# Kernel optimization log

Measured on AMD Instinct MI355X. Metric: run time of the kernel, lower is better.

The kernel has to match this reference:

```python
import jax, jax.numpy as jnp
import numpy as np

N = 100000      # n_nodes
E = 1600000     # n_edges (avg degree 16)
D_IN, D_H, D_OUT = 128, 64, 16


def setup_inputs() -> dict:
    key = jax.random.key(0)
    k1, k2, k3, k4 = jax.random.split(key, 4)
    x = jax.random.normal(k1, (N, D_IN), dtype=jnp.float32)
    edge_index = jax.random.randint(k2, (2, E), 0, N, dtype=jnp.int32)
    W1 = jax.random.normal(k3, (D_IN, D_H), dtype=jnp.float32) / np.sqrt(D_IN)
    b1 = jnp.zeros((D_H,), dtype=jnp.float32)
    W2 = jax.random.normal(k4, (D_H, D_OUT), dtype=jnp.float32) / np.sqrt(D_H)
    b2 = jnp.zeros((D_OUT,), dtype=jnp.float32)
    return {"x": x, "edge_index": edge_index, "W1": W1, "b1": b1, "W2": W2, "b2": b2}


def gcn_conv(x, src, dst, W, b, n):
    """PyG GCNConv: linear transform, then deg^-1/2 A deg^-1/2 aggregation, + bias.
    src/dst already include self-loops."""
    h = x @ W                                              # [n, d_out]
    deg = jax.ops.segment_sum(jnp.ones_like(dst, dtype=h.dtype), dst, num_segments=n)
    dinv = jnp.where(deg > 0, jax.lax.rsqrt(jnp.maximum(deg, 1.0)), 0.0)
    norm = dinv[src] * dinv[dst]                           # [E+n]
    msgs = h[src] * norm[:, None]                          # gather + scale
    out = jax.ops.segment_sum(msgs, dst, num_segments=n)   # scatter-add
    return out + b


def reference(x, edge_index, W1, b1, W2, b2):
    loops = jnp.arange(N, dtype=edge_index.dtype)
    src = jnp.concatenate([edge_index[0], loops])
    dst = jnp.concatenate([edge_index[1], loops])
    h = jax.nn.relu(gcn_conv(x, src, dst, W1, b1, N))
    return gcn_conv(h, src, dst, W2, b2, N)
```

## Files before the change

kernel.cpp:

```cpp
#include <hip/hip_runtime.h>
#include <cstdint>

#define N_NODES 100000
#define N_EDGES 1600000
#define D_IN    128
#define D_H     64
#define D_OUT   16
#define M_TILES 6250

#define NBKT   512
#define NPB    196
#define BCAP   4096
#define TILE_E 4096
#define NTILES ((N_EDGES + TILE_E - 1) / TILE_E)
#define G1     256
#define GEMM_BLOCKS ((M_TILES + 3) / 4)

typedef __attribute__((ext_vector_type(8))) short short8;
typedef __attribute__((ext_vector_type(4))) float floatx4;

static __device__ __forceinline__ unsigned short f2bf(float f) {
    unsigned int u = __float_as_uint(f);
    u = u + 0x7FFFu + ((u >> 16) & 1u);
    return (unsigned short)(u >> 16);
}
static __device__ __forceinline__ float bf2f(unsigned short h) {
    return __uint_as_float(((unsigned int)h) << 16);
}


__global__ __launch_bounds__(512) void zero_small_kernel(int* __restrict__ cursors,
                                                         int* __restrict__ srcs) {
    cursors[threadIdx.x] = 0;
    if (threadIdx.x < 16) srcs[N_EDGES + threadIdx.x] = 0;
}

__global__ __launch_bounds__(256) void fused_bin_gemm1_kernel(
        const int* __restrict__ src, const int* __restrict__ dst,
        int* __restrict__ cursors, int* __restrict__ region,
        const float* __restrict__ x, const float* __restrict__ W1,
        unsigned short* __restrict__ hs) {
    __shared__ int hcnt[NBKT];
    __shared__ int hbase[NBKT];
    __shared__ unsigned short bhi_lds[8192];
    __shared__ unsigned short blo_lds[8192];

    const int t = threadIdx.x;

    if (blockIdx.x < G1) {
        for (int tile = blockIdx.x; tile < NTILES; tile += G1) {
            for (int i = t; i < NBKT; i += 256) hcnt[i] = 0;
            __syncthreads();
            int e0 = tile * TILE_E + t * 16;
            int pk[16], bk[16], rk[16];
            bool full = (e0 + 16 <= N_EDGES);
            if (full) {
                const int4* dp = (const int4*)(dst + e0);
                const int4* sp = (const int4*)(src + e0);
                int dv[16], sv[16];
                #pragma unroll
                for (int q = 0; q < 4; ++q) {
                    int4 d4 = dp[q]; int4 s4 = sp[q];
                    dv[4*q+0]=d4.x; dv[4*q+1]=d4.y; dv[4*q+2]=d4.z; dv[4*q+3]=d4.w;
                    sv[4*q+0]=s4.x; sv[4*q+1]=s4.y; sv[4*q+2]=s4.z; sv[4*q+3]=s4.w;
                }
                #pragma unroll
                for (int k = 0; k < 16; ++k) {
                    int d = dv[k];
                    int b = d / NPB;
                    bk[k] = b;
                    pk[k] = ((d - b * NPB) << 17) | sv[k];
                    rk[k] = atomicAdd(&hcnt[b], 1);
                }
            }
            __syncthreads();
            for (int i = t; i < NBKT; i += 256) {
                int c = hcnt[i];
                if (c > 0) hbase[i] = atomicAdd(&cursors[i], c);
            }
            __syncthreads();
            if (full) {
                #pragma unroll
                for (int k = 0; k < 16; ++k)
                    region[bk[k] * BCAP + hbase[bk[k]] + rk[k]] = pk[k];
            }
            __syncthreads();
        }
        return;
    }

    for (int e = t; e < 8192; e += 256) {
        int j    = e & 7;
        int lane = (e >> 3) & 63;
        int pair = e >> 9;
        int kc   = pair >> 2;
        int nt   = pair & 3;
        int k = kc * 32 + (lane >> 4) * 8 + j;
        int n = nt * 16 + (lane & 15);
        float w = W1[k * D_H + n];
        unsigned short hi = f2bf(w);
        float lo = w - bf2f(hi);
        bhi_lds[e] = hi;
        blo_lds[e] = f2bf(lo);
    }
    __syncthreads();

    int wid  = t >> 6;
    int lane = t & 63;
    int quad = lane >> 4;
    int m    = lane & 15;

    int tile = (blockIdx.x - G1) * 4 + wid;
    if (tile >= M_TILES) return;
    int mbase = tile * 16;

    const float* xr = x + (size_t)(mbase + m) * D_IN + quad * 8;
    short8 ahi[4], alo[4];
    #pragma unroll
    for (int kc = 0; kc < 4; ++kc) {
        floatx4 v0 = *(const floatx4*)(xr + kc * 32);
        floatx4 v1 = *(const floatx4*)(xr + kc * 32 + 4);
        float f[8] = {v0.x, v0.y, v0.z, v0.w, v1.x, v1.y, v1.z, v1.w};
        #pragma unroll
        for (int j = 0; j < 8; ++j) {
            unsigned short hi = f2bf(f[j]);
            float lo = f[j] - bf2f(hi);
            ahi[kc][j] = (short)hi;
            alo[kc][j] = (short)f2bf(lo);
        }
    }

    floatx4 acc[4] = {{0.f,0.f,0.f,0.f},{0.f,0.f,0.f,0.f},{0.f,0.f,0.f,0.f},{0.f,0.f,0.f,0.f}};
    #pragma unroll
    for (int kc = 0; kc < 4; ++kc) {
        #pragma unroll
        for (int nt = 0; nt < 4; ++nt) {
            int fo = ((kc * 4 + nt) * 64 + lane) * 8;
            short8 bhi = *(const short8*)&bhi_lds[fo];
            short8 blo = *(const short8*)&blo_lds[fo];
            acc[nt] = __builtin_amdgcn_mfma_f32_16x16x32_bf16(ahi[kc], bhi, acc[nt], 0, 0, 0);
            acc[nt] = __builtin_amdgcn_mfma_f32_16x16x32_bf16(ahi[kc], blo, acc[nt], 0, 0, 0);
            acc[nt] = __builtin_amdgcn_mfma_f32_16x16x32_bf16(alo[kc], bhi, acc[nt], 0, 0, 0);
        }
    }

    #pragma unroll
    for (int nt = 0; nt < 4; ++nt) {
        int col = nt * 16 + m;
        #pragma unroll
        for (int r = 0; r < 4; ++r) {
            int row = mbase + quad * 4 + r;
            hs[row * D_H + col] = f2bf(acc[nt][r]);
        }
    }
}

__global__ __launch_bounds__(256) void build_kernel(const int* __restrict__ cursors,
                                                    const int* __restrict__ region,
                                                    int* __restrict__ offsets,
                                                    float* __restrict__ dinv,
                                                    int* __restrict__ srcs) {
    __shared__ int lhist[NPB];
    __shared__ int lscan[NPB + 1];
    __shared__ int sbuf[256];
    __shared__ int srt[BCAP];
    __shared__ int red[4];
    int b = blockIdx.x;
    int t = threadIdx.x;

    int c0 = cursors[t];
    int c1 = cursors[t + 256];
    int p = ((t < b) ? c0 : 0) + ((t + 256 < b) ? c1 : 0);
    int lane = t & 63, wid = t >> 6;
    #pragma unroll
    for (int off = 32; off > 0; off >>= 1) p += __shfl_down(p, off);
    if (lane == 0) red[wid] = p;
    __syncthreads();
    int base = red[0] + red[1] + red[2] + red[3];
    int cnt = cursors[b];
    const int* reg = region + b * BCAP;

    for (int i = t; i < NPB; i += 256) lhist[i] = 0;
    __syncthreads();
    for (int i = t; i < cnt; i += 256) {
        int ln = reg[i] >> 17;
        atomicAdd(&lhist[ln], 1);
    }
    __syncthreads();
    int v = (t < NPB) ? lhist[t] : 0;
    sbuf[t] = v;
    __syncthreads();
    for (int off = 1; off < 256; off <<= 1) {
        int u = (t >= off) ? sbuf[t - off] : 0;
        __syncthreads();
        sbuf[t] += u;
        __syncthreads();
    }
    int incl = sbuf[t];
    if (t < NPB) lscan[t] = incl - v;
    if (t == NPB - 1) lscan[NPB] = incl;
    __syncthreads();
    if (t < NPB) lhist[t] = incl - v;
    __syncthreads();

    int node0 = b * NPB;
    int nlim = N_NODES - node0;
    if (nlim > NPB) nlim = NPB;
    if (t < nlim) {
        offsets[node0 + t] = base + lscan[t];
        int c = lscan[t + 1] - lscan[t];
        dinv[node0 + t] = rsqrtf((float)c + 1.0f);
    }
    if (b == (N_NODES - 1) / NPB && t == 0) offsets[N_NODES] = base + cnt;

    for (int i = t; i < cnt; i += 256) {
        int pk = reg[i];
        int ln = pk >> 17;
        int pos = atomicAdd(&lhist[ln], 1);
        srt[pos] = pk & 0x1FFFF;
    }
    __syncthreads();
    for (int i = t; i < cnt; i += 256) srcs[base + i] = srt[i];
}

__global__ __launch_bounds__(256) void agg1_fused_kernel(const unsigned short* __restrict__ hs,
                                                         const int* __restrict__ offsets,
                                                         const int* __restrict__ srcs,
                                                         const float* __restrict__ dinv,
                                                         const float* __restrict__ b1,
                                                         const float* __restrict__ W2,
                                                         float* __restrict__ h2s) {
    __shared__ float w2t[16 * 68];
    __shared__ float rbuf[16 * 68];

    const int tid = threadIdx.x;
    for (int i = tid; i < 1024; i += 256) {
        int j = i >> 4, c = i & 15;
        w2t[c * 68 + j] = W2[i];
    }

    const int g    = tid >> 4;
    const int sl   = tid & 15;
    const int node = blockIdx.x * 16 + g;
    const int c4   = sl * 4;

    const int beg = offsets[node];
    const int end = offsets[node + 1];
    const float dv = dinv[node];

    ushort4 s4v = *(const ushort4*)(hs + (size_t)node * D_H + c4);
    float a0 = bf2f(s4v.x) * dv, a1 = bf2f(s4v.y) * dv;
    float a2 = bf2f(s4v.z) * dv, a3 = bf2f(s4v.w) * dv;

    for (int e = beg; e < end; e += 16) {
        int rem = end - e;
        int idx = srcs[e + sl];
        float dvv = dinv[idx];
        #pragma unroll
        for (int k = 0; k < 16; ++k) {
            int j   = __shfl(idx, k, 16);
            float dj = __shfl(dvv, k, 16);
            ushort4 v = *(const ushort4*)(hs + (size_t)j * D_H + c4);
            float m = (k < rem) ? dj : 0.0f;
            a0 = fmaf(bf2f(v.x), m, a0);
            a1 = fmaf(bf2f(v.y), m, a1);
            a2 = fmaf(bf2f(v.z), m, a2);
            a3 = fmaf(bf2f(v.w), m, a3);
        }
    }

    const floatx4 bb = *(const floatx4*)(b1 + c4);
    float* rb = rbuf + g * 68;
    rb[c4 + 0] = fmaxf(a0 * dv + bb.x, 0.f);
    rb[c4 + 1] = fmaxf(a1 * dv + bb.y, 0.f);
    rb[c4 + 2] = fmaxf(a2 * dv + bb.z, 0.f);
    rb[c4 + 3] = fmaxf(a3 * dv + bb.w, 0.f);
    __syncthreads();

    float p = 0.f;
    #pragma unroll
    for (int t4 = 0; t4 < 16; ++t4) {
        floatx4 rv = *(const floatx4*)(rb + 4 * t4);
        floatx4 wv = *(const floatx4*)(&w2t[sl * 68 + 4 * t4]);
        p += rv.x * wv.x + rv.y * wv.y + rv.z * wv.z + rv.w * wv.w;
    }
    h2s[node * D_OUT + sl] = p * dv;
}

__global__ __launch_bounds__(256) void agg2_kernel(const float* __restrict__ h2s,
                                                   const int* __restrict__ offsets,
                                                   const int* __restrict__ srcs,
                                                   const float* __restrict__ dinv,
                                                   const float* __restrict__ b2,
                                                   float* __restrict__ out) {
    int col = threadIdx.x & 15;
    int nidx = (blockIdx.x * blockDim.x + threadIdx.x) >> 4;
    int stride = (gridDim.x * blockDim.x) >> 4;
    for (int node = nidx; node < N_NODES; node += stride) {
        int beg = offsets[node], end = offsets[node + 1];
        float acc = h2s[node * D_OUT + col];
        for (int e = beg; e < end; e += 16) {
            int rem = end - e;
            const int* ep = srcs + e;
            int jj[16];
            #pragma unroll
            for (int k = 0; k < 16; ++k) jj[k] = ep[k];
            float vv[16];
            #pragma unroll
            for (int k = 0; k < 16; ++k) vv[k] = h2s[jj[k] * D_OUT + col];
            #pragma unroll
            for (int k = 0; k < 16; ++k) {
                float m = (k < rem) ? 1.0f : 0.0f;
                acc = fmaf(vv[k], m, acc);
            }
        }
        out[node * D_OUT + col] = acc * dinv[node] + b2[col];
    }
}

extern "C" void kernel_launch(void* const* d_in, const int* in_sizes, int n_in,
                              void* d_out, int out_size, void* d_ws, size_t ws_size,
                              hipStream_t stream) {
    const float* x  = (const float*)d_in[0];
    const int*   ei = (const int*)d_in[1];
    const float* W1 = (const float*)d_in[2];
    const float* b1 = (const float*)d_in[3];
    const float* W2 = (const float*)d_in[4];
    const float* b2 = (const float*)d_in[5];
    float* out = (float*)d_out;

    const int* src = ei;
    const int* dst = ei + N_EDGES;

    char* w = (char*)d_ws;
    int*   cursors  = (int*)(w + 0);
    int*   offsets  = (int*)(w + 4096);
    float* dinv     = (float*)(w + 404224);
    int*   srcs     = (int*)(w + 804224);
    unsigned short* hs = (unsigned short*)(w + 7204352);
    float* h2s      = (float*)(w + 20004480);
    int*   region   = (int*)(w + 26404480);

    zero_small_kernel<<<1, 512, 0, stream>>>(cursors, srcs);
    fused_bin_gemm1_kernel<<<G1 + GEMM_BLOCKS, 256, 0, stream>>>(
        src, dst, cursors, region, x, W1, hs);
    build_kernel<<<NBKT, 256, 0, stream>>>(cursors, region, offsets, dinv, srcs);
    agg1_fused_kernel<<<6250, 256, 0, stream>>>(hs, offsets, srcs, dinv, b1, W2, h2s);
    agg2_kernel<<<6250, 256, 0, stream>>>(h2s, offsets, srcs, dinv, b2, out);
}
```

Measured before the change: 209.8 us.

## Prescale GEMM1 output by source dinv using a separate atomic degree pass

Result: slower. 257.9 us (+22.9%).

```diff
diff --git a/kernel.cpp b/kernel.cpp
--- a/kernel.cpp
+++ b/kernel.cpp
@@ -29,17 +29,32 @@
 }
 
 
-__global__ __launch_bounds__(512) void zero_small_kernel(int* __restrict__ cursors,
-                                                         int* __restrict__ srcs) {
-    cursors[threadIdx.x] = 0;
-    if (threadIdx.x < 16) srcs[N_EDGES + threadIdx.x] = 0;
+__global__ __launch_bounds__(256) void zero_kernel(int* __restrict__ cursors,
+                                                   int* __restrict__ srcs,
+                                                   int* __restrict__ deg) {
+    int gid = blockIdx.x * 256 + threadIdx.x;
+    if (gid < N_NODES) deg[gid] = 0;
+    if (gid < NBKT) cursors[gid] = 0;
+    if (gid < 16) srcs[N_EDGES + gid] = 0;
+}
+
+__global__ __launch_bounds__(256) void deg_kernel(const int* __restrict__ dst,
+                                                  int* __restrict__ deg) {
+    int i = blockIdx.x * 256 + threadIdx.x;
+    if (i < N_EDGES / 4) {
+        int4 d = ((const int4*)dst)[i];
+        atomicAdd(&deg[d.x], 1);
+        atomicAdd(&deg[d.y], 1);
+        atomicAdd(&deg[d.z], 1);
+        atomicAdd(&deg[d.w], 1);
+    }
 }
 
 __global__ __launch_bounds__(256) void fused_bin_gemm1_kernel(
         const int* __restrict__ src, const int* __restrict__ dst,
         int* __restrict__ cursors, int* __restrict__ region,
         const float* __restrict__ x, const float* __restrict__ W1,
-        unsigned short* __restrict__ hs) {
+        const int* __restrict__ deg, unsigned short* __restrict__ hs) {
     __shared__ int hcnt[NBKT];
     __shared__ int hbase[NBKT];
     __shared__ unsigned short bhi_lds[8192];
@@ -144,13 +159,17 @@
         }
     }
 
+    float dv[4];
+    #pragma unroll
+    for (int r = 0; r < 4; ++r)
+        dv[r] = rsqrtf((float)deg[mbase + quad * 4 + r] + 1.0f);
     #pragma unroll
     for (int nt = 0; nt < 4; ++nt) {
         int col = nt * 16 + m;
         #pragma unroll
         for (int r = 0; r < 4; ++r) {
             int row = mbase + quad * 4 + r;
-            hs[row * D_H + col] = f2bf(acc[nt][r]);
+            hs[row * D_H + col] = f2bf(acc[nt][r] * dv[r]);
         }
     }
 }
@@ -246,22 +265,18 @@
 
     const int beg = offsets[node];
     const int end = offsets[node + 1];
-    const float dv = dinv[node];
 
     ushort4 s4v = *(const ushort4*)(hs + (size_t)node * D_H + c4);
-    float a0 = bf2f(s4v.x) * dv, a1 = bf2f(s4v.y) * dv;
-    float a2 = bf2f(s4v.z) * dv, a3 = bf2f(s4v.w) * dv;
+    float a0 = bf2f(s4v.x), a1 = bf2f(s4v.y), a2 = bf2f(s4v.z), a3 = bf2f(s4v.w);
 
     for (int e = beg; e < end; e += 16) {
         int rem = end - e;
         int idx = srcs[e + sl];
-        float dvv = dinv[idx];
         #pragma unroll
         for (int k = 0; k < 16; ++k) {
-            int j   = __shfl(idx, k, 16);
-            float dj = __shfl(dvv, k, 16);
+            int j = __shfl(idx, k, 16);
             ushort4 v = *(const ushort4*)(hs + (size_t)j * D_H + c4);
-            float m = (k < rem) ? dj : 0.0f;
+            float m = (k < rem) ? 1.0f : 0.0f;
             a0 = fmaf(bf2f(v.x), m, a0);
             a1 = fmaf(bf2f(v.y), m, a1);
             a2 = fmaf(bf2f(v.z), m, a2);
@@ -269,6 +284,7 @@
         }
     }
 
+    const float dv = dinv[node];
     const floatx4 bb = *(const floatx4*)(b1 + c4);
     float* rb = rbuf + g * 68;
     rb[c4 + 0] = fmaxf(a0 * dv + bb.x, 0.f);
@@ -340,10 +356,12 @@
     unsigned short* hs = (unsigned short*)(w + 7204352);
     float* h2s      = (float*)(w + 20004480);
     int*   region   = (int*)(w + 26404480);
-
-    zero_small_kernel<<<1, 512, 0, stream>>>(cursors, srcs);
+    int*   deg      = (int*)(w + 34793088);
+
+    zero_kernel<<<391, 256, 0, stream>>>(cursors, srcs, deg);
+    deg_kernel<<<1563, 256, 0, stream>>>(dst, deg);
     fused_bin_gemm1_kernel<<<G1 + GEMM_BLOCKS, 256, 0, stream>>>(
-        src, dst, cursors, region, x, W1, hs);
+        src, dst, cursors, region, x, W1, deg, hs);
     build_kernel<<<NBKT, 256, 0, stream>>>(cursors, region, offsets, dinv, srcs);
     agg1_fused_kernel<<<6250, 256, 0, stream>>>(hs, offsets, srcs, dinv, b1, W2, h2s);
     agg2_kernel<<<6250, 256, 0, stream>>>(h2s, offsets, srcs, dinv, b2, out);
```
